# Performance work log

Hardware: AMD Instinct MI355X
Metric: run time of the kernel (lower is better)

Reference implementation:

```python
import jax, jax.numpy as jnp
import numpy as np

N, E = 10000, 160000
F_IN, H1, C1, C2 = 256, 8, 128, 128
SLOPE = 0.2  # PyG GATConv default negative_slope


def setup_inputs() -> dict:
    key = jax.random.key(0)
    ks = jax.random.split(key, 9)
    s = 0.05
    return {
        "x": jax.random.normal(ks[0], (N, F_IN), jnp.float32),
        "edge_index": jax.random.randint(ks[1], (2, E), 0, N),
        "W1": jax.random.normal(ks[2], (F_IN, H1 * C1), jnp.float32) * s,
        "a_src1": jax.random.normal(ks[3], (H1, C1), jnp.float32) * s,
        "a_dst1": jax.random.normal(ks[4], (H1, C1), jnp.float32) * s,
        "b1": jnp.zeros((H1 * C1,), jnp.float32),
        "W2": jax.random.normal(ks[5], (H1 * C1, C2), jnp.float32) * s,
        "a_src2": jax.random.normal(ks[6], (1, C2), jnp.float32) * s,
        "a_dst2": jax.random.normal(ks[7], (1, C2), jnp.float32) * s,
        "b2": jnp.zeros((C2,), jnp.float32),
    }


def gat_conv(x, src, dst, W, a_s, a_d, b, heads, out_ch, concat):
    n = x.shape[0]
    h = (x @ W).reshape(n, heads, out_ch)            # [N,H,C]
    s_src = jnp.einsum("nhc,hc->nh", h, a_s)         # [N,H]
    s_dst = jnp.einsum("nhc,hc->nh", h, a_d)
    e = jax.nn.leaky_relu(s_src[src] + s_dst[dst], SLOPE)   # [Etot,H]
    # segment softmax over incoming edges per destination (self-loops guarantee non-empty segments)
    m = jax.lax.stop_gradient(jax.ops.segment_max(e, dst, num_segments=n))
    p = jnp.exp(e - m[dst])
    denom = jax.ops.segment_sum(p, dst, num_segments=n)
    alpha = p / denom[dst]                            # [Etot,H]
    out = jax.ops.segment_sum(h[src] * alpha[:, :, None], dst, num_segments=n)  # [N,H,C]
    out = out.reshape(n, heads * out_ch) if concat else out.mean(axis=1)
    return out + b


def reference(x, edge_index, W1, a_src1, a_dst1, b1, W2, a_src2, a_dst2, b2):
    n = x.shape[0]
    loops = jnp.arange(n, dtype=edge_index.dtype)     # PyG add_self_loops=True
    src = jnp.concatenate([edge_index[0], loops])
    dst = jnp.concatenate([edge_index[1], loops])
    # dropout layers are identity at inference (training=False)
    h1 = jax.nn.elu(gat_conv(x, src, dst, W1, a_src1, a_dst1, b1, H1, C1, True))
    return gat_conv(h1, src, dst, W2, a_src2, a_dst2, b2, 1, C2, False)
```

## Files before the change

### kernel.cpp

```cpp
#include <hip/hip_runtime.h>
#include <math.h>

#define F_IN 256
#define H1 8
#define C1 128
#define HC1 1024
#define C2 128
#define SLOPE 0.2f

typedef unsigned short u16;
typedef __attribute__((ext_vector_type(8))) short bf16x8;
typedef __attribute__((ext_vector_type(4))) float f32x4;


__device__ __forceinline__ float lrelu(float v) { return v > 0.f ? v : SLOPE * v; }

__device__ __forceinline__ unsigned bf16_rne(float x) {
    unsigned u = __float_as_uint(x);
    u += 0x7fffu + ((u >> 16) & 1u);
    return u >> 16;
}

__device__ __forceinline__ void split2(float a, float b, unsigned& hi, unsigned& lo) {
    unsigned ha = bf16_rne(a), hb = bf16_rne(b);
    float fa = __uint_as_float(ha << 16), fb = __uint_as_float(hb << 16);
    hi = ha | (hb << 16);
    lo = bf16_rne(a - fa) | (bf16_rne(b - fb) << 16);
}

__device__ __forceinline__ void gload16(const u16* g, u16* l) {
    __builtin_amdgcn_global_load_lds(
        (const __attribute__((address_space(1))) unsigned*)g,
        (__attribute__((address_space(3))) unsigned*)l, 16, 0, 0);
}


__global__ void hist_kernel(const int* __restrict__ dst, int* __restrict__ deg, int E) {
    int i = blockIdx.x * blockDim.x + threadIdx.x;
    if (i < E) atomicAdd(&deg[dst[i]], 1);
}

__global__ void scan_kernel(const int* __restrict__ deg, int* __restrict__ start,
                            int* __restrict__ cursor, int n) {
    __shared__ int wsum[16];
    __shared__ int wpre[16];
    __shared__ int ctot;
    const int tid = threadIdx.x;
    const int lane = tid & 63, wv = tid >> 6;
    int carry = 0;
    for (int base = 0; base < n; base += 1024) {
        int i = base + tid;
        int v = (i < n) ? deg[i] : 0;
        int x = v;
#pragma unroll
        for (int o = 1; o < 64; o <<= 1) {
            int y = __shfl_up(x, o);
            if (lane >= o) x += y;
        }
        if (lane == 63) wsum[wv] = x;
        __syncthreads();
        if (tid < 16) {
            int s = wsum[tid];
            int xx = s;
#pragma unroll
            for (int o = 1; o < 16; o <<= 1) {
                int y = __shfl_up(xx, o);
                if (tid >= o) xx += y;
            }
            wpre[tid] = xx - s;
            if (tid == 15) ctot = xx;
        }
        __syncthreads();
        int excl = carry + wpre[wv] + (x - v);
        if (i < n) { start[i] = excl; cursor[i] = excl; }
        carry += ctot;
        __syncthreads();
    }
    if (tid == 0) start[n] = carry;
}

__global__ void scatter_kernel(const int* __restrict__ src, const int* __restrict__ dst,
                               int* __restrict__ cursor, int* __restrict__ ssorted,
                               unsigned char* __restrict__ rowloc,
                               int E, int N) {
    int i = blockIdx.x * blockDim.x + threadIdx.x;
    if (i < E) {
        int d = dst[i];
        int pos = atomicAdd(&cursor[d], 1);
        ssorted[pos] = src[i];
        rowloc[pos] = (unsigned char)(d & 15);
    } else if (i < E + N) {
        int d = i - E;
        int pos = atomicAdd(&cursor[d], 1);
        ssorted[pos] = d;
        rowloc[pos] = (unsigned char)(d & 15);
    }
}


__global__ void split_mat_deg(const float* __restrict__ in, u16* __restrict__ hi,
                              u16* __restrict__ lo, int n,
                              int* __restrict__ deg, int nd) {
    int i = blockIdx.x * blockDim.x + threadIdx.x;
    if (i < nd) deg[i] = 1;
    if (i >= n) return;
    float v = in[i];
    unsigned h = bf16_rne(v);
    hi[i] = (u16)h;
    lo[i] = (u16)bf16_rne(v - __uint_as_float(h << 16));
}

__global__ void split_transpose2(const float* __restrict__ in1, u16* __restrict__ hi1,
                                 u16* __restrict__ lo1, int R1, int Cc1,
                                 const float* __restrict__ in2, u16* __restrict__ hi2,
                                 u16* __restrict__ lo2, int R2, int Cc2) {
    int i = blockIdx.x * blockDim.x + threadIdx.x;
    int n1 = R1 * Cc1;
    if (i < n1) {
        int r = i / Cc1, c = i % Cc1;
        float v = in1[i];
        unsigned h = bf16_rne(v);
        hi1[(size_t)c * R1 + r] = (u16)h;
        lo1[(size_t)c * R1 + r] = (u16)bf16_rne(v - __uint_as_float(h << 16));
    } else {
        int j = i - n1;
        if (j >= R2 * Cc2) return;
        int r = j / Cc2, c = j % Cc2;
        float v = in2[j];
        unsigned h = bf16_rne(v);
        hi2[(size_t)c * R2 + r] = (u16)h;
        lo2[(size_t)c * R2 + r] = (u16)bf16_rne(v - __uint_as_float(h << 16));
    }
}


__global__ __launch_bounds__(256) void gemm_mfma(const u16* __restrict__ Ahi,
                                                 const u16* __restrict__ Alo,
                                                 const u16* __restrict__ Bhi,
                                                 const u16* __restrict__ Blo,
                                                 u16* __restrict__ Cbf,
                                                 int M, int N, int K,
                                                 const float* __restrict__ a_s,
                                                 const float* __restrict__ a_d,
                                                 float* __restrict__ ssrc,
                                                 float* __restrict__ sdst) {
    __shared__ u16 lds[16384];
    const int t = threadIdx.x;
    const int rbase = blockIdx.y * 128;
    const int cbase = blockIdx.x * 128;

    const int lane = t & 63;
    const int R0 = (t >> 7) << 6;
    const int C0 = ((t >> 6) & 1) << 6;
    const int lrow = lane & 15;
    const int kq = lane >> 4;

    f32x4 acc[4][4] = {};

    for (int k0 = 0; k0 < K; k0 += 32) {
#pragma unroll
        for (int i = 0; i < 2; i++) {
            int c = t + (i << 8);
            int row = c >> 2;
            int kc = (c & 3) << 3;
            int ar = min(rbase + row, M - 1);
            int br = cbase + row;
            gload16(Ahi + (size_t)ar * K + k0 + kc, &lds[c * 8]);
            gload16(Alo + (size_t)ar * K + k0 + kc, &lds[4096 + c * 8]);
            gload16(Bhi + (size_t)br * K + k0 + kc, &lds[8192 + c * 8]);
            gload16(Blo + (size_t)br * K + k0 + kc, &lds[12288 + c * 8]);
        }
        __syncthreads();

        bf16x8 ah[4], al[4], bh[4], bl[4];
#pragma unroll
        for (int m = 0; m < 4; m++) {
            int off = (R0 + (m << 4) + lrow) * 32 + (kq << 3);
            ah[m] = *(const bf16x8*)&lds[off];
            al[m] = *(const bf16x8*)&lds[4096 + off];
        }
#pragma unroll
        for (int n = 0; n < 4; n++) {
            int off = (C0 + (n << 4) + lrow) * 32 + (kq << 3);
            bh[n] = *(const bf16x8*)&lds[8192 + off];
            bl[n] = *(const bf16x8*)&lds[12288 + off];
        }
#pragma unroll
        for (int m = 0; m < 4; m++)
#pragma unroll
            for (int n = 0; n < 4; n++) {
                acc[m][n] = __builtin_amdgcn_mfma_f32_16x16x32_bf16(ah[m], bh[n], acc[m][n], 0, 0, 0);
                acc[m][n] = __builtin_amdgcn_mfma_f32_16x16x32_bf16(ah[m], bl[n], acc[m][n], 0, 0, 0);
                acc[m][n] = __builtin_amdgcn_mfma_f32_16x16x32_bf16(al[m], bh[n], acc[m][n], 0, 0, 0);
            }
        __syncthreads();
    }

#pragma unroll
    for (int m = 0; m < 4; m++)
#pragma unroll
        for (int n = 0; n < 4; n++) {
            int col = cbase + C0 + (n << 4) + lrow;
#pragma unroll
            for (int r = 0; r < 4; r++) {
                int row = rbase + R0 + (m << 4) + kq * 4 + r;
                if (row < M) Cbf[(size_t)row * N + col] = (u16)bf16_rne(acc[m][n][r]);
            }
        }

    {
        float* fl = (float*)lds;
        const int head = blockIdx.x;
        const int c01 = (t >> 6) & 1;
        float asv[4], adv[4];
#pragma unroll
        for (int n = 0; n < 4; n++) {
            int col = head * 128 + C0 + (n << 4) + lrow;
            asv[n] = a_s[col];
            adv[n] = a_d[col];
        }
#pragma unroll
        for (int m = 0; m < 4; m++)
#pragma unroll
            for (int r = 0; r < 4; r++) {
                float vs = 0.f, vd = 0.f;
#pragma unroll
                for (int n = 0; n < 4; n++) {
                    float h = acc[m][n][r];
                    vs += asv[n] * h;
                    vd += adv[n] * h;
                }
#pragma unroll
                for (int o = 1; o < 16; o <<= 1) {
                    vs += __shfl_xor(vs, o);
                    vd += __shfl_xor(vd, o);
                }
                if (lrow == 0) {
                    int lr = R0 + (m << 4) + kq * 4 + r;
                    fl[c01 * 128 + lr] = vs;
                    fl[256 + c01 * 128 + lr] = vd;
                }
            }
        __syncthreads();
        if (t < 128) {
            int row = rbase + t;
            if (row < M) {
                ssrc[row * H1 + head] = fl[t] + fl[128 + t];
                sdst[row * H1 + head] = fl[256 + t] + fl[384 + t];
            }
        }
    }
}


__global__ __launch_bounds__(256) void gemm_mfma64(const u16* __restrict__ Ahi,
                                                   const u16* __restrict__ Alo,
                                                   const u16* __restrict__ Bhi,
                                                   const u16* __restrict__ Blo,
                                                   u16* __restrict__ Cbf,
                                                   int M, int N, int K) {
    __shared__ u16 lds[16384];
    const int t = threadIdx.x;
    const int rbase = blockIdx.y * 64;
    const int cbase = blockIdx.x * 64;

    const int lane = t & 63;
    const int w = t >> 6;
    const int R0 = (w >> 1) << 5;
    const int C0 = (w & 1) << 5;
    const int lrow = lane & 15;
    const int kq = lane >> 4;

    f32x4 acc[2][2] = {};

    for (int k0 = 0; k0 < K; k0 += 64) {
        {
            int row = (w << 4) + (lane >> 2);
            int kcc = (lane & 3) << 3;
            int ar = min(rbase + row, M - 1);
            int br = cbase + row;
            const size_t ga = (size_t)ar * K + k0 + kcc;
            const size_t gb = (size_t)br * K + k0 + kcc;
            const int ldo = row * 32 + kcc;
#pragma unroll
            for (int s2 = 0; s2 < 2; s2++) {
                gload16(Ahi + ga + s2 * 32, &lds[s2 * 2048 + ldo]);
                gload16(Alo + ga + s2 * 32, &lds[4096 + s2 * 2048 + ldo]);
                gload16(Bhi + gb + s2 * 32, &lds[8192 + s2 * 2048 + ldo]);
                gload16(Blo + gb + s2 * 32, &lds[12288 + s2 * 2048 + ldo]);
            }
        }
        __syncthreads();

#pragma unroll
        for (int s = 0; s < 2; s++) {
            bf16x8 ah[2], al[2], bh[2], bl[2];
#pragma unroll
            for (int m = 0; m < 2; m++) {
                int off = s * 2048 + (R0 + (m << 4) + lrow) * 32 + (kq << 3);
                ah[m] = *(const bf16x8*)&lds[off];
                al[m] = *(const bf16x8*)&lds[4096 + off];
            }
#pragma unroll
            for (int n = 0; n < 2; n++) {
                int off = s * 2048 + (C0 + (n << 4) + lrow) * 32 + (kq << 3);
                bh[n] = *(const bf16x8*)&lds[8192 + off];
                bl[n] = *(const bf16x8*)&lds[12288 + off];
            }
#pragma unroll
            for (int m = 0; m < 2; m++)
#pragma unroll
                for (int n = 0; n < 2; n++) {
                    acc[m][n] = __builtin_amdgcn_mfma_f32_16x16x32_bf16(ah[m], bh[n], acc[m][n], 0, 0, 0);
                    acc[m][n] = __builtin_amdgcn_mfma_f32_16x16x32_bf16(ah[m], bl[n], acc[m][n], 0, 0, 0);
                    acc[m][n] = __builtin_amdgcn_mfma_f32_16x16x32_bf16(al[m], bh[n], acc[m][n], 0, 0, 0);
                }
        }
        __syncthreads();
    }

#pragma unroll
    for (int m = 0; m < 2; m++)
#pragma unroll
        for (int n = 0; n < 2; n++) {
            int col = cbase + C0 + (n << 4) + lrow;
#pragma unroll
            for (int r = 0; r < 4; r++) {
                int row = rbase + R0 + (m << 4) + kq * 4 + r;
                if (row < M) Cbf[(size_t)row * N + col] = (u16)bf16_rne(acc[m][n][r]);
            }
        }
}


__global__ __launch_bounds__(256) void scores2_bf(const unsigned* __restrict__ hbf,
                                                  const float* __restrict__ a_s,
                                                  const float* __restrict__ a_d,
                                                  float* __restrict__ ssrc,
                                                  float* __restrict__ sdst, int N) {
    int n = blockIdx.x * 4 + (threadIdx.x >> 6);
    if (n >= N) return;
    int lane = threadIdx.x & 63;
    unsigned u = hbf[(size_t)n * 64 + lane];
    float c0 = __uint_as_float(u << 16);
    float c1 = __uint_as_float(u & 0xffff0000u);
    float vs = c0 * a_s[2 * lane] + c1 * a_s[2 * lane + 1];
    float vd = c0 * a_d[2 * lane] + c1 * a_d[2 * lane + 1];
    for (int off = 32; off; off >>= 1) {
        vs += __shfl_xor(vs, off);
        vd += __shfl_xor(vd, off);
    }
    if (lane == 0) { ssrc[n] = vs; sdst[n] = vd; }
}


__global__ __launch_bounds__(256) void softmax_edges1(
    const float* __restrict__ ssrc, const float* __restrict__ sdst,
    const int* __restrict__ start, const int* __restrict__ ssorted,
    float* __restrict__ alphab, int N, int ET) {
    int lane = threadIdx.x & 63;
    int p = lane & 15, g = lane >> 4;
    int task = (blockIdx.x * 4 + (threadIdx.x >> 6)) * 4 + g;
    if (task >= N * H1) return;
    int d = task >> 3, hh = task & 7;
    int s0 = start[d], ne = start[d + 1] - s0;
    float sd = sdst[d * H1 + hh];
    int src0 = 0; float v0 = -1e30f;
    if (p < ne) { src0 = ssorted[s0 + p]; v0 = lrelu(ssrc[src0 * H1 + hh] + sd); }
    float m = v0;
    for (int e = p + 16; e < ne; e += 16)
        m = fmaxf(m, lrelu(ssrc[ssorted[s0 + e] * H1 + hh] + sd));
    for (int o = 8; o; o >>= 1) m = fmaxf(m, __shfl_xor(m, o));
    float p0 = (p < ne) ? __expf(v0 - m) : 0.f;
    float s = p0;
    for (int e = p + 16; e < ne; e += 16)
        s += __expf(lrelu(ssrc[ssorted[s0 + e] * H1 + hh] + sd) - m);
    for (int o = 8; o; o >>= 1) s += __shfl_xor(s, o);
    float inv = 1.f / s;
    float* ab = alphab + (size_t)hh * ET;
    if (p < ne) ab[s0 + p] = p0 * inv;
    for (int e = p + 16; e < ne; e += 16)
        ab[s0 + e] = __expf(lrelu(ssrc[ssorted[s0 + e] * H1 + hh] + sd) - m) * inv;
}


__global__ __launch_bounds__(256) void agg_mfma1(
    const u16* __restrict__ hbf,
    const float* __restrict__ alphab,
    const unsigned char* __restrict__ rowloc,
    const int* __restrict__ start,
    const int* __restrict__ ssorted,
    const float* __restrict__ bias,
    u16* __restrict__ outHi, u16* __restrict__ outLo,
    int N, int ET) {
    __shared__ unsigned A32[2][16 * 68];
    __shared__ int mOff[2][64];

    const int hh = blockIdx.x & 7;
    const int g = blockIdx.x >> 3;
    const int t = threadIdx.x;
    const int w = t >> 6;
    const int lane = t & 63;
    const int cl = lane & 15, q = lane >> 4;

    const int d0 = g * 16;
    const int e0 = start[d0], e1 = start[min(d0 + 16, N)];
    const float* ab = alphab + (size_t)hh * ET;

    const int lanebyte = hh * 256 + w * 64 + 4 * cl;
    const char* hbase = (const char*)hbf;

    const int nk = (e1 - e0 + 63) >> 6;

    auto fill = [&](int b, int kb) {
        unsigned* Az = &A32[b][(lane >> 2) * 68 + (lane & 3) * 16];
        uint4 z = {0u, 0u, 0u, 0u};
        *(uint4*)(Az) = z;
        *(uint4*)(Az + 4) = z;
        *(uint4*)(Az + 8) = z;
        *(uint4*)(Az + 12) = z;
        int pos = kb + lane;
        bool valid = pos < e1;
        int ps = valid ? pos : e0;
        float af = valid ? ab[ps] : 0.f;
        unsigned ahiu = bf16_rne(af);
        unsigned alou = bf16_rne(af - __uint_as_float(ahiu << 16));
        int rr = rowloc[ps];
        mOff[b][lane] = ssorted[ps] << 11;
        asm volatile("s_waitcnt lgkmcnt(0)" ::: "memory");
        A32[b][rr * 68 + lane] = ahiu | (alou << 16);
    };

    f32x4 acc0 = {}, acc1 = {};

    if (w == 0 && nk > 0) fill(0, e0);

    for (int i = 0; i < nk; ++i) {
        __syncthreads();
        const int b = i & 1;
        if (w == 0 && i + 1 < nk) fill(b ^ 1, e0 + (i + 1) * 64);

        const int mb = q * 8;
        int4 o0 = *(const int4*)&mOff[b][mb];
        int4 o1 = *(const int4*)&mOff[b][mb + 4];
        int4 o2 = *(const int4*)&mOff[b][32 + mb];
        int4 o3 = *(const int4*)&mOff[b][32 + mb + 4];
        int oo[16] = {o0.x, o0.y, o0.z, o0.w, o1.x, o1.y, o1.z, o1.w,
                      o2.x, o2.y, o2.z, o2.w, o3.x, o3.y, o3.z, o3.w};

        unsigned gld[16];
#pragma unroll
        for (int j = 0; j < 16; j++)
            gld[j] = *(const unsigned*)(hbase + (unsigned)(oo[j] + lanebyte));

        const unsigned* Ar = &A32[b][cl * 68 + mb];
        uint4 a0 = *(const uint4*)(Ar);
        uint4 a1 = *(const uint4*)(Ar + 4);
        uint4 a2 = *(const uint4*)(Ar + 32);
        uint4 a3 = *(const uint4*)(Ar + 36);
        unsigned aw[16] = {a0.x, a0.y, a0.z, a0.w, a1.x, a1.y, a1.z, a1.w,
                           a2.x, a2.y, a2.z, a2.w, a3.x, a3.y, a3.z, a3.w};

        union { unsigned u[4]; bf16x8 v; } ahi0, alo0, ahi1, alo1, b00, b10, b01, b11;
#pragma unroll
        for (int r = 0; r < 4; r++) {
            ahi0.u[r] = __builtin_amdgcn_perm(aw[2 * r + 1], aw[2 * r], 0x05040100u);
            alo0.u[r] = __builtin_amdgcn_perm(aw[2 * r + 1], aw[2 * r], 0x07060302u);
            ahi1.u[r] = __builtin_amdgcn_perm(aw[8 + 2 * r + 1], aw[8 + 2 * r], 0x05040100u);
            alo1.u[r] = __builtin_amdgcn_perm(aw[8 + 2 * r + 1], aw[8 + 2 * r], 0x07060302u);
            b00.u[r] = __builtin_amdgcn_perm(gld[2 * r + 1], gld[2 * r], 0x05040100u);
            b10.u[r] = __builtin_amdgcn_perm(gld[2 * r + 1], gld[2 * r], 0x07060302u);
            b01.u[r] = __builtin_amdgcn_perm(gld[8 + 2 * r + 1], gld[8 + 2 * r], 0x05040100u);
            b11.u[r] = __builtin_amdgcn_perm(gld[8 + 2 * r + 1], gld[8 + 2 * r], 0x07060302u);
        }

        acc0 = __builtin_amdgcn_mfma_f32_16x16x32_bf16(ahi0.v, b00.v, acc0, 0, 0, 0);
        acc0 = __builtin_amdgcn_mfma_f32_16x16x32_bf16(alo0.v, b00.v, acc0, 0, 0, 0);
        acc1 = __builtin_amdgcn_mfma_f32_16x16x32_bf16(ahi0.v, b10.v, acc1, 0, 0, 0);
        acc1 = __builtin_amdgcn_mfma_f32_16x16x32_bf16(alo0.v, b10.v, acc1, 0, 0, 0);
        acc0 = __builtin_amdgcn_mfma_f32_16x16x32_bf16(ahi1.v, b01.v, acc0, 0, 0, 0);
        acc0 = __builtin_amdgcn_mfma_f32_16x16x32_bf16(alo1.v, b01.v, acc0, 0, 0, 0);
        acc1 = __builtin_amdgcn_mfma_f32_16x16x32_bf16(ahi1.v, b11.v, acc1, 0, 0, 0);
        acc1 = __builtin_amdgcn_mfma_f32_16x16x32_bf16(alo1.v, b11.v, acc1, 0, 0, 0);
    }

    {
        int chbase = w * 32 + 2 * cl;
        float bv0 = bias[hh * C1 + chbase];
        float bv1 = bias[hh * C1 + chbase + 1];
#pragma unroll
        for (int r = 0; r < 4; r++) {
            int d = d0 + q * 4 + r;
            if (d >= N) continue;
            float v0 = acc0[r] + bv0;
            float v1 = acc1[r] + bv1;
            v0 = v0 > 0.f ? v0 : expm1f(v0);
            v1 = v1 > 0.f ? v1 : expm1f(v1);
            unsigned hi, lo;
            split2(v0, v1, hi, lo);
            size_t idx = (size_t)d * HC1 + hh * C1 + chbase;
            ((unsigned*)outHi)[idx >> 1] = hi;
            ((unsigned*)outLo)[idx >> 1] = lo;
        }
    }
}


template<int H, bool SPLITOUT>
__global__ __launch_bounds__(256) void agg_bf(const unsigned* __restrict__ hbf,
                                              const float* __restrict__ ssrc,
                                              const float* __restrict__ sdst,
                                              const int* __restrict__ start,
                                              const int* __restrict__ ssorted,
                                              const float* __restrict__ bias,
                                              float* __restrict__ out,
                                              unsigned* __restrict__ outHi,
                                              unsigned* __restrict__ outLo, int N) {
    int hh, grp;
    if (H == 8) { hh = blockIdx.x & 7; grp = blockIdx.x >> 3; }
    else        { hh = 0;              grp = blockIdx.x; }
    int wid = threadIdx.x >> 6, lane = threadIdx.x & 63;
    int d = grp * 4 + wid;
    if (d >= N) return;
    const int g = lane >> 4, p = lane & 15;
    int s0 = start[d];
    int ne = start[d + 1] - s0;
    float sd = sdst[d * H + hh];

    const unsigned* hlane = hbf + hh * 64 + p * 4;
    const int rowstride = H * 64;

    int src0 = 0; float v0 = -1e30f;
    if (lane < ne) { src0 = ssorted[s0 + lane]; v0 = lrelu(ssrc[src0 * H + hh] + sd); }
    float m = v0;
    for (int e = lane + 64; e < ne; e += 64)
        m = fmaxf(m, lrelu(ssrc[ssorted[s0 + e] * H + hh] + sd));
    for (int o = 32; o; o >>= 1) m = fmaxf(m, __shfl_xor(m, o));

    float p0 = (lane < ne) ? __expf(v0 - m) : 0.f;
    float ssum = p0;
    for (int e = lane + 64; e < ne; e += 64)
        ssum += __expf(lrelu(ssrc[ssorted[s0 + e] * H + hh] + sd) - m);
    for (int o = 32; o; o >>= 1) ssum += __shfl_xor(ssum, o);
    float inv = 1.f / ssum;

    float acc[8] = {};
    for (int base = 0; base < ne; base += 64) {
        int srcr; float al;
        if (base == 0) { srcr = src0; al = p0 * inv; }
        else {
            srcr = 0; al = 0.f;
            int e = base + lane;
            if (e < ne) {
                srcr = ssorted[s0 + e];
                al = __expf(lrelu(ssrc[srcr * H + hh] + sd) - m) * inv;
            }
        }
        int cnt = min(64, ne - base);
        for (int e2 = 0; e2 < cnt; e2 += 4) {
            float a = __shfl(al, e2 + g);
            int sr = __shfl(srcr, e2 + g);
            uint4 u = *(const uint4*)(hlane + (size_t)sr * rowstride);
            acc[0] += a * __uint_as_float(u.x << 16);
            acc[1] += a * __uint_as_float(u.x & 0xffff0000u);
            acc[2] += a * __uint_as_float(u.y << 16);
            acc[3] += a * __uint_as_float(u.y & 0xffff0000u);
            acc[4] += a * __uint_as_float(u.z << 16);
            acc[5] += a * __uint_as_float(u.z & 0xffff0000u);
            acc[6] += a * __uint_as_float(u.w << 16);
            acc[7] += a * __uint_as_float(u.w & 0xffff0000u);
        }
    }

#pragma unroll
    for (int i = 0; i < 8; i++) {
        acc[i] += __shfl_xor(acc[i], 16);
        acc[i] += __shfl_xor(acc[i], 32);
    }

    float r0 = g == 0 ? acc[0] : g == 1 ? acc[2] : g == 2 ? acc[4] : acc[6];
    float r1 = g == 0 ? acc[1] : g == 1 ? acc[3] : g == 2 ? acc[5] : acc[7];
    int j = 4 * p + g;
    float2 bv = ((const float2*)bias)[hh * 64 + j];
    r0 += bv.x; r1 += bv.y;
    size_t idx = (size_t)d * (H * 64) + hh * 64 + j;
    if (SPLITOUT) {
        r0 = r0 > 0.f ? r0 : expm1f(r0);
        r1 = r1 > 0.f ? r1 : expm1f(r1);
        unsigned hi, lo;
        split2(r0, r1, hi, lo);
        outHi[idx] = hi;
        outLo[idx] = lo;
    } else {
        ((float2*)out)[idx] = make_float2(r0, r1);
    }
}


extern "C" void kernel_launch(void* const* d_in, const int* in_sizes, int n_in,
                              void* d_out, int out_size, void* d_ws, size_t ws_size,
                              hipStream_t stream) {
    const float* x      = (const float*)d_in[0];
    const int*   ei     = (const int*)d_in[1];
    const float* W1     = (const float*)d_in[2];
    const float* a_src1 = (const float*)d_in[3];
    const float* a_dst1 = (const float*)d_in[4];
    const float* b1     = (const float*)d_in[5];
    const float* W2     = (const float*)d_in[6];
    const float* a_src2 = (const float*)d_in[7];
    const float* a_dst2 = (const float*)d_in[8];
    const float* b2     = (const float*)d_in[9];
    float* out = (float*)d_out;

    int E = in_sizes[1] / 2;
    int N = in_sizes[0] / F_IN;
    int ET = E + N;
    const int* esrc = ei;
    const int* edst = ei + E;

    char* ws = (char*)d_ws;
    size_t off = 0;
    auto alloc = [&](size_t bytes) -> char* {
        char* p = ws + off;
        off = (off + bytes + 255) & ~(size_t)255;
        return p;
    };
    u16* x_hi    = (u16*)alloc((size_t)N * F_IN * 2);
    u16* x_lo    = (u16*)alloc((size_t)N * F_IN * 2);
    u16* W1t_hi  = (u16*)alloc((size_t)F_IN * HC1 * 2);
    u16* W1t_lo  = (u16*)alloc((size_t)F_IN * HC1 * 2);
    u16* W2t_hi  = (u16*)alloc((size_t)HC1 * C2 * 2);
    u16* W2t_lo  = (u16*)alloc((size_t)HC1 * C2 * 2);
    u16* h1_bf   = (u16*)alloc((size_t)N * HC1 * 2);
    u16* h1a_hi  = (u16*)alloc((size_t)N * HC1 * 2);
    u16* h1a_lo  = (u16*)alloc((size_t)N * HC1 * 2);
    u16* h2_bf   = (u16*)alloc((size_t)N * C2 * 2);
    float* ss1   = (float*)alloc((size_t)N * H1 * 4);
    float* sd1   = (float*)alloc((size_t)N * H1 * 4);
    float* ss2   = (float*)alloc((size_t)N * 4);
    float* sd2   = (float*)alloc((size_t)N * 4);
    int* deg     = (int*)alloc((size_t)N * 4);
    int* startp  = (int*)alloc((size_t)(N + 1) * 4);
    int* cursor  = (int*)alloc((size_t)N * 4);
    int* ssorted = (int*)alloc((size_t)ET * 4);
    unsigned char* rowloc = (unsigned char*)alloc((size_t)ET);
    float* alpha1 = (float*)x_hi;

    split_mat_deg<<<(N * F_IN + 255) / 256, 256, 0, stream>>>(x, x_hi, x_lo, N * F_IN, deg, N);
    hist_kernel<<<(E + 255) / 256, 256, 0, stream>>>(edst, deg, E);
    scan_kernel<<<1, 1024, 0, stream>>>(deg, startp, cursor, N);
    scatter_kernel<<<(E + N + 255) / 256, 256, 0, stream>>>(esrc, edst, cursor, ssorted, rowloc, E, N);

    split_transpose2<<<(F_IN * HC1 + HC1 * C2 + 255) / 256, 256, 0, stream>>>(
        W1, W1t_hi, W1t_lo, F_IN, HC1, W2, W2t_hi, W2t_lo, HC1, C2);

    gemm_mfma<<<dim3(HC1 / 128, (N + 127) / 128), 256, 0, stream>>>(
        x_hi, x_lo, W1t_hi, W1t_lo, h1_bf, N, HC1, F_IN, a_src1, a_dst1, ss1, sd1);
    softmax_edges1<<<(N * H1 + 15) / 16, 256, 0, stream>>>(
        ss1, sd1, startp, ssorted, alpha1, N, ET);
    agg_mfma1<<<((N + 15) / 16) * H1, 256, 0, stream>>>(
        h1_bf, alpha1, rowloc, startp, ssorted, b1, h1a_hi, h1a_lo, N, ET);

    gemm_mfma64<<<dim3(C2 / 64, (N + 63) / 64), 256, 0, stream>>>(
        h1a_hi, h1a_lo, W2t_hi, W2t_lo, h2_bf, N, C2, HC1);
    scores2_bf<<<(N + 3) / 4, 256, 0, stream>>>(
        (const unsigned*)h2_bf, a_src2, a_dst2, ss2, sd2, N);
    agg_bf<1, false><<<(N + 3) / 4, 256, 0, stream>>>(
        (const unsigned*)h2_bf, ss2, sd2, startp, ssorted, b2,
        out, nullptr, nullptr, N);
}
```

Baseline: 229.4 us.

## Split aggregation edges across warp pairs with wider gathers and LDS reduction

Reassigns the four warps in the layer-1 MFMA aggregation kernel so each warp covers half the edges of a 64-edge chunk and half the channels, instead of all edges for a quarter of the channels. Each lane now gathers 8-byte neighbor feature words instead of 4-byte ones, halving the number of gather instructions per warp, and keeps four accumulators. Partial sums from the two edge halves are combined through shared memory before the bias/ELU epilogue, which also writes 8-byte output words. This adds an extra synchronization and an LDS reduction at the end, and puts more accumulator registers in each thread.

```diff
diff --git a/kernel.cpp b/kernel.cpp
--- a/kernel.cpp
+++ b/kernel.cpp
@@ -402,12 +402,14 @@
     const int w = t >> 6;
     const int lane = t & 63;
     const int cl = lane & 15, q = lane >> 4;
+    const int chhalf = w & 1;
+    const int ehalf = w >> 1;
 
     const int d0 = g * 16;
     const int e0 = start[d0], e1 = start[min(d0 + 16, N)];
     const float* ab = alphab + (size_t)hh * ET;
 
-    const int lanebyte = hh * 256 + w * 64 + 4 * cl;
+    const int lanebyte = hh * 256 + chhalf * 128 + 8 * cl;
     const char* hbase = (const char*)hbf;
 
     const int nk = (e1 - e0 + 63) >> 6;
@@ -431,7 +433,7 @@
         A32[b][rr * 68 + lane] = ahiu | (alou << 16);
     };
 
-    f32x4 acc0 = {}, acc1 = {};
+    f32x4 acc0 = {}, acc1 = {}, acc2 = {}, acc3 = {};
 
     if (w == 0 && nk > 0) fill(0, e0);
 
@@ -441,66 +443,83 @@
         if (w == 0 && i + 1 < nk) fill(b ^ 1, e0 + (i + 1) * 64);
 
         const int mb = q * 8;
-        int4 o0 = *(const int4*)&mOff[b][mb];
-        int4 o1 = *(const int4*)&mOff[b][mb + 4];
-        int4 o2 = *(const int4*)&mOff[b][32 + mb];
-        int4 o3 = *(const int4*)&mOff[b][32 + mb + 4];
-        int oo[16] = {o0.x, o0.y, o0.z, o0.w, o1.x, o1.y, o1.z, o1.w,
-                      o2.x, o2.y, o2.z, o2.w, o3.x, o3.y, o3.z, o3.w};
-
-        unsigned gld[16];
-#pragma unroll
-        for (int j = 0; j < 16; j++)
-            gld[j] = *(const unsigned*)(hbase + (unsigned)(oo[j] + lanebyte));
-
-        const unsigned* Ar = &A32[b][cl * 68 + mb];
+        const int eb = ehalf * 32;
+        int4 o0 = *(const int4*)&mOff[b][eb + mb];
+        int4 o1 = *(const int4*)&mOff[b][eb + mb + 4];
+        int oo[8] = {o0.x, o0.y, o0.z, o0.w, o1.x, o1.y, o1.z, o1.w};
+
+        uint2 gld[8];
+#pragma unroll
+        for (int j = 0; j < 8; j++)
+            gld[j] = *(const uint2*)(hbase + (unsigned)(oo[j] + lanebyte));
+
+        const unsigned* Ar = &A32[b][cl * 68 + eb + mb];
         uint4 a0 = *(const uint4*)(Ar);
         uint4 a1 = *(const uint4*)(Ar + 4);
-        uint4 a2 = *(const uint4*)(Ar + 32);
-        uint4 a3 = *(const uint4*)(Ar + 36);
-        unsigned aw[16] = {a0.x, a0.y, a0.z, a0.w, a1.x, a1.y, a1.z, a1.w,
-                           a2.x, a2.y, a2.z, a2.w, a3.x, a3.y, a3.z, a3.w};
-
-        union { unsigned u[4]; bf16x8 v; } ahi0, alo0, ahi1, alo1, b00, b10, b01, b11;
+        unsigned aw[8] = {a0.x, a0.y, a0.z, a0.w, a1.x, a1.y, a1.z, a1.w};
+
+        union { unsigned u[4]; bf16x8 v; } ahi, alo, b0, b1, b2, b3;
 #pragma unroll
         for (int r = 0; r < 4; r++) {
-            ahi0.u[r] = __builtin_amdgcn_perm(aw[2 * r + 1], aw[2 * r], 0x05040100u);
-            alo0.u[r] = __builtin_amdgcn_perm(aw[2 * r + 1], aw[2 * r], 0x07060302u);
-            ahi1.u[r] = __builtin_amdgcn_perm(aw[8 + 2 * r + 1], aw[8 + 2 * r], 0x05040100u);
-            alo1.u[r] = __builtin_amdgcn_perm(aw[8 + 2 * r + 1], aw[8 + 2 * r], 0x07060302u);
-            b00.u[r] = __builtin_amdgcn_perm(gld[2 * r + 1], gld[2 * r], 0x05040100u);
-            b10.u[r] = __builtin_amdgcn_perm(gld[2 * r + 1], gld[2 * r], 0x07060302u);
-            b01.u[r] = __builtin_amdgcn_perm(gld[8 + 2 * r + 1], gld[8 + 2 * r], 0x05040100u);
-            b11.u[r] = __builtin_amdgcn_perm(gld[8 + 2 * r + 1], gld[8 + 2 * r], 0x07060302u);
-        }
-
-        acc0 = __builtin_amdgcn_mfma_f32_16x16x32_bf16(ahi0.v, b00.v, acc0, 0, 0, 0);
-        acc0 = __builtin_amdgcn_mfma_f32_16x16x32_bf16(alo0.v, b00.v, acc0, 0, 0, 0);
-        acc1 = __builtin_amdgcn_mfma_f32_16x16x32_bf16(ahi0.v, b10.v, acc1, 0, 0, 0);
-        acc1 = __builtin_amdgcn_mfma_f32_16x16x32_bf16(alo0.v, b10.v, acc1, 0, 0, 0);
-        acc0 = __builtin_amdgcn_mfma_f32_16x16x32_bf16(ahi1.v, b01.v, acc0, 0, 0, 0);
-        acc0 = __builtin_amdgcn_mfma_f32_16x16x32_bf16(alo1.v, b01.v, acc0, 0, 0, 0);
-        acc1 = __builtin_amdgcn_mfma_f32_16x16x32_bf16(ahi1.v, b11.v, acc1, 0, 0, 0);
-        acc1 = __builtin_amdgcn_mfma_f32_16x16x32_bf16(alo1.v, b11.v, acc1, 0, 0, 0);
-    }
-
+            ahi.u[r] = __builtin_amdgcn_perm(aw[2 * r + 1], aw[2 * r], 0x05040100u);
+            alo.u[r] = __builtin_amdgcn_perm(aw[2 * r + 1], aw[2 * r], 0x07060302u);
+            b0.u[r] = __builtin_amdgcn_perm(gld[2 * r + 1].x, gld[2 * r].x, 0x05040100u);
+            b1.u[r] = __builtin_amdgcn_perm(gld[2 * r + 1].x, gld[2 * r].x, 0x07060302u);
+            b2.u[r] = __builtin_amdgcn_perm(gld[2 * r + 1].y, gld[2 * r].y, 0x05040100u);
+            b3.u[r] = __builtin_amdgcn_perm(gld[2 * r + 1].y, gld[2 * r].y, 0x07060302u);
+        }
+
+        acc0 = __builtin_amdgcn_mfma_f32_16x16x32_bf16(ahi.v, b0.v, acc0, 0, 0, 0);
+        acc0 = __builtin_amdgcn_mfma_f32_16x16x32_bf16(alo.v, b0.v, acc0, 0, 0, 0);
+        acc1 = __builtin_amdgcn_mfma_f32_16x16x32_bf16(ahi.v, b1.v, acc1, 0, 0, 0);
+        acc1 = __builtin_amdgcn_mfma_f32_16x16x32_bf16(alo.v, b1.v, acc1, 0, 0, 0);
+        acc2 = __builtin_amdgcn_mfma_f32_16x16x32_bf16(ahi.v, b2.v, acc2, 0, 0, 0);
+        acc2 = __builtin_amdgcn_mfma_f32_16x16x32_bf16(alo.v, b2.v, acc2, 0, 0, 0);
+        acc3 = __builtin_amdgcn_mfma_f32_16x16x32_bf16(ahi.v, b3.v, acc3, 0, 0, 0);
+        acc3 = __builtin_amdgcn_mfma_f32_16x16x32_bf16(alo.v, b3.v, acc3, 0, 0, 0);
+    }
+
+    __syncthreads();
     {
-        int chbase = w * 32 + 2 * cl;
-        float bv0 = bias[hh * C1 + chbase];
-        float bv1 = bias[hh * C1 + chbase + 1];
-#pragma unroll
-        for (int r = 0; r < 4; r++) {
-            int d = d0 + q * 4 + r;
-            if (d >= N) continue;
-            float v0 = acc0[r] + bv0;
-            float v1 = acc1[r] + bv1;
-            v0 = v0 > 0.f ? v0 : expm1f(v0);
-            v1 = v1 > 0.f ? v1 : expm1f(v1);
-            unsigned hi, lo;
-            split2(v0, v1, hi, lo);
-            size_t idx = (size_t)d * HC1 + hh * C1 + chbase;
-            ((unsigned*)outHi)[idx >> 1] = hi;
-            ((unsigned*)outLo)[idx >> 1] = lo;
+        float* CMB = (float*)A32;
+        float av[16] = {acc0[0], acc0[1], acc0[2], acc0[3],
+                        acc1[0], acc1[1], acc1[2], acc1[3],
+                        acc2[0], acc2[1], acc2[2], acc2[3],
+                        acc3[0], acc3[1], acc3[2], acc3[3]};
+        if (ehalf == 1) {
+            float* dp = CMB + chhalf * 1088 + lane;
+#pragma unroll
+            for (int v = 0; v < 16; v++) dp[v * 68] = av[v];
+        }
+        __syncthreads();
+        if (ehalf == 0) {
+            const float* sp = CMB + chhalf * 1088 + lane;
+#pragma unroll
+            for (int v = 0; v < 16; v++) av[v] += sp[v * 68];
+            int chbase = chhalf * 64 + 4 * cl;
+            float bv0 = bias[hh * C1 + chbase];
+            float bv1 = bias[hh * C1 + chbase + 1];
+            float bv2 = bias[hh * C1 + chbase + 2];
+            float bv3 = bias[hh * C1 + chbase + 3];
+#pragma unroll
+            for (int r = 0; r < 4; r++) {
+                int d = d0 + q * 4 + r;
+                if (d >= N) continue;
+                float v0 = av[r] + bv0;
+                float v1 = av[4 + r] + bv1;
+                float v2 = av[8 + r] + bv2;
+                float v3 = av[12 + r] + bv3;
+                v0 = v0 > 0.f ? v0 : expm1f(v0);
+                v1 = v1 > 0.f ? v1 : expm1f(v1);
+                v2 = v2 > 0.f ? v2 : expm1f(v2);
+                v3 = v3 > 0.f ? v3 : expm1f(v3);
+                unsigned h01, l01, h23, l23;
+                split2(v0, v1, h01, l01);
+                split2(v2, v3, h23, l23);
+                size_t idx = (size_t)d * HC1 + hh * C1 + chbase;
+                ((uint2*)outHi)[idx >> 2] = make_uint2(h01, h23);
+                ((uint2*)outLo)[idx >> 2] = make_uint2(l01, l23);
+            }
         }
     }
 }
```

New measurement: 232.8 us. No clear change (+1.5%).
